# Kernel optimization log

Measured on AMD Instinct MI355X. Metric: run time of the kernel, lower is better.

The kernel has to match this reference:

```python
import jax, jax.numpy as jnp
import numpy as np


def setup_inputs() -> dict:
    key = jax.random.key(0)
    k1, k2 = jax.random.split(key)
    B, N, T, D = 16, 2048, 168, 64
    spatial_nodes = jax.random.normal(k1, (B, N, D), dtype=jnp.float32)
    temporal_nodes = jax.random.normal(k2, (B, T, D), dtype=jnp.float32)
    return {"spatial_nodes": spatial_nodes, "temporal_nodes": temporal_nodes}


def reference(spatial_nodes, temporal_nodes):
    # node_embs: [B, N+T, D]
    node_embs = jnp.concatenate([spatial_nodes, temporal_nodes], axis=1)
    # Dense pairwise similarity, then tanh(relu(.)) threshold.
    # batch_adj: [B, N+T, N+T]
    batch_adj = jnp.einsum('bnf,bmf->bnm', node_embs, node_embs)
    batch_adj = jnp.tanh(jax.nn.relu(batch_adj))
    # The torch module additionally extracts per-batch variable-length
    # edge lists (nonzero indices + weights) from batch_adj; those are a
    # pure re-indexing of batch_adj with data-dependent shapes, so the
    # jit-compatible reference returns the dense adjacency, from which
    # edge lists are trivially recoverable (nonzero entries of batch_adj).
    return batch_adj
```

## Files before the change

### kernel.cpp

```cpp
#include <hip/hip_runtime.h>
#include <stdint.h>


constexpr int Bsz = 16;
constexpr int Nsp = 2048;
constexpr int Ttm = 168;
constexpr int D   = 64;
constexpr int M   = Nsp + Ttm;
constexpr int TILE = 128;
constexpr int NT   = (M + TILE - 1) / TILE;
constexpr int NPAIR = NT * (NT + 1) / 2;
constexpr int LROW = 72;
constexpr int TROW = 132;

typedef __attribute__((ext_vector_type(8)))  short bf16x8;
typedef __attribute__((ext_vector_type(16))) float f32x16;

__device__ inline void split_bf16(float x, unsigned short& h, unsigned short& l) {
    union { float f; uint32_t u; } a; a.f = x;
    uint32_t hu = (a.u + 0x7FFFu + ((a.u >> 16) & 1u)) >> 16;
    h = (unsigned short)hu;
    union { uint32_t u; float f; } hf; hf.u = hu << 16;
    union { float f; uint32_t u; } r; r.f = x - hf.f;
    uint32_t lu = (r.u + 0x7FFFu + ((r.u >> 16) & 1u)) >> 16;
    l = (unsigned short)lu;
}

__device__ inline float act_tanh_relu(float x) {
    const float xr = fmaxf(x, 0.0f);
    const float e  = __expf(2.0f * xr);
    return 1.0f - 2.0f / (e + 1.0f);
}

__global__ __launch_bounds__(256, 2) void stgraph_kernel(
    const float* __restrict__ spatial,
    const float* __restrict__ temporal,
    float* __restrict__ out)
{
    __shared__ __align__(16) unsigned short pool[4 * TILE * LROW];
    unsigned short* Ah = pool;
    unsigned short* Al = pool + 1 * TILE * LROW;
    unsigned short* Bh = pool + 2 * TILE * LROW;
    unsigned short* Bl = pool + 3 * TILE * LROW;
    float* T = (float*)pool;

    const int tid = threadIdx.x;
    const int b   = blockIdx.y;

    const int p = blockIdx.x;
    int ti = (int)((37.0f - sqrtf(1369.0f - 8.0f * (float)p)) * 0.5f);
    while (ti * (37 - ti) / 2 > p) --ti;
    while ((ti + 1) * (36 - ti) / 2 <= p) ++ti;
    const int tj = ti + (p - ti * (37 - ti) / 2);
    const bool diag = (ti == tj);

    const float* sp_b = spatial  + (size_t)b * Nsp * D;
    const float* tp_b = temporal + (size_t)b * Ttm * D;

    #pragma unroll
    for (int it = 0; it < 8; ++it) {
        const int f4  = tid + 256 * it;
        const int row = f4 >> 4;
        const int c4  = f4 & 15;
        const int gi  = ti * TILE + row;
        float4 v = make_float4(0.f, 0.f, 0.f, 0.f);
        if (gi < M) {
            const float* src = (gi < Nsp) ? (sp_b + (size_t)gi * D)
                                          : (tp_b + (size_t)(gi - Nsp) * D);
            v = *(const float4*)(src + c4 * 4);
        }
        unsigned short h[4], l[4];
        split_bf16(v.x, h[0], l[0]); split_bf16(v.y, h[1], l[1]);
        split_bf16(v.z, h[2], l[2]); split_bf16(v.w, h[3], l[3]);
        *(uint2*)(&Ah[row * LROW + c4 * 4]) = *(const uint2*)h;
        *(uint2*)(&Al[row * LROW + c4 * 4]) = *(const uint2*)l;
    }
    if (!diag) {
        #pragma unroll
        for (int it = 0; it < 8; ++it) {
            const int f4  = tid + 256 * it;
            const int row = f4 >> 4;
            const int c4  = f4 & 15;
            const int gj  = tj * TILE + row;
            float4 v = make_float4(0.f, 0.f, 0.f, 0.f);
            if (gj < M) {
                const float* src = (gj < Nsp) ? (sp_b + (size_t)gj * D)
                                              : (tp_b + (size_t)(gj - Nsp) * D);
                v = *(const float4*)(src + c4 * 4);
            }
            unsigned short h[4], l[4];
            split_bf16(v.x, h[0], l[0]); split_bf16(v.y, h[1], l[1]);
            split_bf16(v.z, h[2], l[2]); split_bf16(v.w, h[3], l[3]);
            *(uint2*)(&Bh[row * LROW + c4 * 4]) = *(const uint2*)h;
            *(uint2*)(&Bl[row * LROW + c4 * 4]) = *(const uint2*)l;
        }
    }
    __syncthreads();

    const unsigned short* FBh = diag ? Ah : Bh;
    const unsigned short* FBl = diag ? Al : Bl;

    const int lane = tid & 63;
    const int w    = tid >> 6;
    const int l31  = lane & 31;
    const int lhi  = lane >> 5;
    const int arow = 32 * w + l31;

    f32x16 acc[4] = {};

    #pragma unroll
    for (int ks = 0; ks < 4; ++ks) {
        const int ko = ks * 16 + 8 * lhi;
        bf16x8 ahi = *(const bf16x8*)(&Ah[arow * LROW + ko]);
        bf16x8 alo = *(const bf16x8*)(&Al[arow * LROW + ko]);
        #pragma unroll
        for (int t = 0; t < 4; ++t) {
            const int brow = 32 * t + l31;
            bf16x8 bhi = *(const bf16x8*)(&FBh[brow * LROW + ko]);
            bf16x8 blo = *(const bf16x8*)(&FBl[brow * LROW + ko]);
            acc[t] = __builtin_amdgcn_mfma_f32_32x32x16_bf16(ahi, bhi, acc[t], 0, 0, 0);
            acc[t] = __builtin_amdgcn_mfma_f32_32x32x16_bf16(ahi, blo, acc[t], 0, 0, 0);
            acc[t] = __builtin_amdgcn_mfma_f32_32x32x16_bf16(alo, bhi, acc[t], 0, 0, 0);
        }
    }

    float* out_b = out + (size_t)b * M * M;

    if (!diag) __syncthreads();

    #pragma unroll
    for (int t = 0; t < 4; ++t) {
        const int jl = 32 * t + l31;
        const int gj = tj * TILE + jl;
        float v[16];
        #pragma unroll
        for (int r = 0; r < 16; ++r) v[r] = act_tanh_relu(acc[t][r]);

        if (gj < M) {
            #pragma unroll
            for (int r = 0; r < 16; ++r) {
                const int gi = ti * TILE + 32 * w + (r & 3) + 8 * (r >> 2) + 4 * lhi;
                if (gi < M) out_b[(size_t)gi * M + gj] = v[r];
            }
        }
        if (!diag) {
            #pragma unroll
            for (int g = 0; g < 4; ++g) {
                const int rowbase = 32 * w + 8 * g + 4 * lhi;
                float4 w4 = make_float4(v[4 * g + 0], v[4 * g + 1],
                                        v[4 * g + 2], v[4 * g + 3]);
                *(float4*)(&T[jl * TROW + rowbase]) = w4;
            }
        }
    }

    if (!diag) {
        __syncthreads();
        #pragma unroll
        for (int it = 0; it < 16; ++it) {
            const int slot = tid + 256 * it;
            const int jl   = slot >> 5;
            const int c4   = slot & 31;
            const int grow = tj * TILE + jl;
            if (grow < M) {
                float4 v4 = *(const float4*)(&T[jl * TROW + 4 * c4]);
                *(float4*)(&out_b[(size_t)grow * M + ti * TILE + 4 * c4]) = v4;
            }
        }
    }
}

extern "C" void kernel_launch(void* const* d_in, const int* in_sizes, int n_in,
                              void* d_out, int out_size, void* d_ws, size_t ws_size,
                              hipStream_t stream) {
    const float* spatial  = (const float*)d_in[0];
    const float* temporal = (const float*)d_in[1];
    float* out = (float*)d_out;

    dim3 block(256);
    dim3 grid(NPAIR, Bsz);
    stgraph_kernel<<<grid, block, 0, stream>>>(spatial, temporal, out);
}
```

Baseline: 430.8 us.

## Drop LDS staging; feed MFMA from global loads and store transposed tile directly

Removes all shared-memory staging. Each wave now loads its A and B rows straight from global memory and splits them into bf16 hi/lo pairs in registers. The mirrored (transposed) output tile is written with float4 stores straight from the accumulators instead of going through an LDS transpose. The kernel also uses a hardware reciprocal in the activation and raises the launch-bounds occupancy hint from 2 to 3. The aim is to cut LDS traffic and barriers. The cost is that every wave redundantly loads and splits the same B rows, and the transposed stores scatter 16-byte pieces across many rows, which coalesces poorly.

Result: no change. 425.5 us (-1.2%).

```diff
diff --git a/kernel.cpp b/kernel.cpp
--- a/kernel.cpp
+++ b/kernel.cpp
@@ -10,40 +10,37 @@
 constexpr int TILE = 128;
 constexpr int NT   = (M + TILE - 1) / TILE;
 constexpr int NPAIR = NT * (NT + 1) / 2;
-constexpr int LROW = 72;
-constexpr int TROW = 132;
 
 typedef __attribute__((ext_vector_type(8)))  short bf16x8;
 typedef __attribute__((ext_vector_type(16))) float f32x16;
 
-__device__ inline void split_bf16(float x, unsigned short& h, unsigned short& l) {
-    union { float f; uint32_t u; } a; a.f = x;
-    uint32_t hu = (a.u + 0x7FFFu + ((a.u >> 16) & 1u)) >> 16;
-    h = (unsigned short)hu;
-    union { uint32_t u; float f; } hf; hf.u = hu << 16;
-    union { float f; uint32_t u; } r; r.f = x - hf.f;
-    uint32_t lu = (r.u + 0x7FFFu + ((r.u >> 16) & 1u)) >> 16;
-    l = (unsigned short)lu;
+__device__ inline void split8(const float4& a, const float4& b,
+                              bf16x8& hi, bf16x8& lo) {
+    float x[8] = {a.x, a.y, a.z, a.w, b.x, b.y, b.z, b.w};
+    #pragma unroll
+    for (int i = 0; i < 8; ++i) {
+        union { float f; uint32_t u; } v; v.f = x[i];
+        uint32_t hu = (v.u + 0x7FFFu + ((v.u >> 16) & 1u)) >> 16;
+        union { uint32_t u; float f; } hf; hf.u = hu << 16;
+        union { float f; uint32_t u; } r; r.f = x[i] - hf.f;
+        uint32_t lu = (r.u + 0x7FFFu + ((r.u >> 16) & 1u)) >> 16;
+        hi[i] = (short)hu;
+        lo[i] = (short)lu;
+    }
 }
 
 __device__ inline float act_tanh_relu(float x) {
     const float xr = fmaxf(x, 0.0f);
     const float e  = __expf(2.0f * xr);
-    return 1.0f - 2.0f / (e + 1.0f);
+    const float r  = __builtin_amdgcn_rcpf(e + 1.0f);
+    return 1.0f - 2.0f * r;
 }
 
-__global__ __launch_bounds__(256, 2) void stgraph_kernel(
+__global__ __launch_bounds__(256, 3) void stgraph_kernel(
     const float* __restrict__ spatial,
     const float* __restrict__ temporal,
     float* __restrict__ out)
 {
-    __shared__ __align__(16) unsigned short pool[4 * TILE * LROW];
-    unsigned short* Ah = pool;
-    unsigned short* Al = pool + 1 * TILE * LROW;
-    unsigned short* Bh = pool + 2 * TILE * LROW;
-    unsigned short* Bl = pool + 3 * TILE * LROW;
-    float* T = (float*)pool;
-
     const int tid = threadIdx.x;
     const int b   = blockIdx.y;
 
@@ -57,67 +54,50 @@
     const float* sp_b = spatial  + (size_t)b * Nsp * D;
     const float* tp_b = temporal + (size_t)b * Ttm * D;
 
-    #pragma unroll
-    for (int it = 0; it < 8; ++it) {
-        const int f4  = tid + 256 * it;
-        const int row = f4 >> 4;
-        const int c4  = f4 & 15;
-        const int gi  = ti * TILE + row;
-        float4 v = make_float4(0.f, 0.f, 0.f, 0.f);
-        if (gi < M) {
-            const float* src = (gi < Nsp) ? (sp_b + (size_t)gi * D)
-                                          : (tp_b + (size_t)(gi - Nsp) * D);
-            v = *(const float4*)(src + c4 * 4);
-        }
-        unsigned short h[4], l[4];
-        split_bf16(v.x, h[0], l[0]); split_bf16(v.y, h[1], l[1]);
-        split_bf16(v.z, h[2], l[2]); split_bf16(v.w, h[3], l[3]);
-        *(uint2*)(&Ah[row * LROW + c4 * 4]) = *(const uint2*)h;
-        *(uint2*)(&Al[row * LROW + c4 * 4]) = *(const uint2*)l;
-    }
-    if (!diag) {
-        #pragma unroll
-        for (int it = 0; it < 8; ++it) {
-            const int f4  = tid + 256 * it;
-            const int row = f4 >> 4;
-            const int c4  = f4 & 15;
-            const int gj  = tj * TILE + row;
-            float4 v = make_float4(0.f, 0.f, 0.f, 0.f);
-            if (gj < M) {
-                const float* src = (gj < Nsp) ? (sp_b + (size_t)gj * D)
-                                              : (tp_b + (size_t)(gj - Nsp) * D);
-                v = *(const float4*)(src + c4 * 4);
-            }
-            unsigned short h[4], l[4];
-            split_bf16(v.x, h[0], l[0]); split_bf16(v.y, h[1], l[1]);
-            split_bf16(v.z, h[2], l[2]); split_bf16(v.w, h[3], l[3]);
-            *(uint2*)(&Bh[row * LROW + c4 * 4]) = *(const uint2*)h;
-            *(uint2*)(&Bl[row * LROW + c4 * 4]) = *(const uint2*)l;
-        }
-    }
-    __syncthreads();
-
-    const unsigned short* FBh = diag ? Ah : Bh;
-    const unsigned short* FBl = diag ? Al : Bl;
-
     const int lane = tid & 63;
     const int w    = tid >> 6;
     const int l31  = lane & 31;
     const int lhi  = lane >> 5;
-    const int arow = 32 * w + l31;
+
+    const int giA = ti * TILE + 32 * w + l31;
+    const float* rowA = nullptr;
+    if (giA < M)
+        rowA = (giA < Nsp) ? sp_b + (size_t)giA * D
+                           : tp_b + (size_t)(giA - Nsp) * D;
+
+    const float* rowB[4];
+    #pragma unroll
+    for (int t = 0; t < 4; ++t) {
+        const int gj = tj * TILE + 32 * t + l31;
+        rowB[t] = nullptr;
+        if (gj < M)
+            rowB[t] = (gj < Nsp) ? sp_b + (size_t)gj * D
+                                 : tp_b + (size_t)(gj - Nsp) * D;
+    }
 
     f32x16 acc[4] = {};
 
     #pragma unroll
     for (int ks = 0; ks < 4; ++ks) {
         const int ko = ks * 16 + 8 * lhi;
-        bf16x8 ahi = *(const bf16x8*)(&Ah[arow * LROW + ko]);
-        bf16x8 alo = *(const bf16x8*)(&Al[arow * LROW + ko]);
+
+        float4 a0 = make_float4(0.f, 0.f, 0.f, 0.f), a1 = a0;
+        if (rowA) {
+            a0 = *(const float4*)(rowA + ko);
+            a1 = *(const float4*)(rowA + ko + 4);
+        }
+        bf16x8 ahi, alo;
+        split8(a0, a1, ahi, alo);
+
         #pragma unroll
         for (int t = 0; t < 4; ++t) {
-            const int brow = 32 * t + l31;
-            bf16x8 bhi = *(const bf16x8*)(&FBh[brow * LROW + ko]);
-            bf16x8 blo = *(const bf16x8*)(&FBl[brow * LROW + ko]);
+            float4 b0 = make_float4(0.f, 0.f, 0.f, 0.f), b1 = b0;
+            if (rowB[t]) {
+                b0 = *(const float4*)(rowB[t] + ko);
+                b1 = *(const float4*)(rowB[t] + ko + 4);
+            }
+            bf16x8 bhi, blo;
+            split8(b0, b1, bhi, blo);
             acc[t] = __builtin_amdgcn_mfma_f32_32x32x16_bf16(ahi, bhi, acc[t], 0, 0, 0);
             acc[t] = __builtin_amdgcn_mfma_f32_32x32x16_bf16(ahi, blo, acc[t], 0, 0, 0);
             acc[t] = __builtin_amdgcn_mfma_f32_32x32x16_bf16(alo, bhi, acc[t], 0, 0, 0);
@@ -126,12 +106,9 @@
 
     float* out_b = out + (size_t)b * M * M;
 
-    if (!diag) __syncthreads();
-
     #pragma unroll
     for (int t = 0; t < 4; ++t) {
-        const int jl = 32 * t + l31;
-        const int gj = tj * TILE + jl;
+        const int gj = tj * TILE + 32 * t + l31;
         float v[16];
         #pragma unroll
         for (int r = 0; r < 16; ++r) v[r] = act_tanh_relu(acc[t][r]);
@@ -142,29 +119,14 @@
                 const int gi = ti * TILE + 32 * w + (r & 3) + 8 * (r >> 2) + 4 * lhi;
                 if (gi < M) out_b[(size_t)gi * M + gj] = v[r];
             }
-        }
-        if (!diag) {
-            #pragma unroll
-            for (int g = 0; g < 4; ++g) {
-                const int rowbase = 32 * w + 8 * g + 4 * lhi;
-                float4 w4 = make_float4(v[4 * g + 0], v[4 * g + 1],
-                                        v[4 * g + 2], v[4 * g + 3]);
-                *(float4*)(&T[jl * TROW + rowbase]) = w4;
-            }
-        }
-    }
-
-    if (!diag) {
-        __syncthreads();
-        #pragma unroll
-        for (int it = 0; it < 16; ++it) {
-            const int slot = tid + 256 * it;
-            const int jl   = slot >> 5;
-            const int c4   = slot & 31;
-            const int grow = tj * TILE + jl;
-            if (grow < M) {
-                float4 v4 = *(const float4*)(&T[jl * TROW + 4 * c4]);
-                *(float4*)(&out_b[(size_t)grow * M + ti * TILE + 4 * c4]) = v4;
+            if (!diag) {
+                #pragma unroll
+                for (int g = 0; g < 4; ++g) {
+                    const int gibase = ti * TILE + 32 * w + 8 * g + 4 * lhi;
+                    float4 w4 = make_float4(v[4 * g + 0], v[4 * g + 1],
+                                            v[4 * g + 2], v[4 * g + 3]);
+                    *(float4*)(&out_b[(size_t)gj * M + gibase]) = w4;
+                }
             }
         }
     }
```
